# Kernel optimization log

Measured on AMD Instinct MI355X. Metric: run time of the kernel, lower is better.

The kernel has to match this reference:

```python
import jax, jax.numpy as jnp
import numpy as np

HID = 1024
HEADS = 16
HEAD_DIM = HID // HEADS
NEG = -10000000000.0


def setup_inputs() -> dict:
    key = jax.random.key(0)
    ks = jax.random.split(key, 12)
    B, S = 4, 2048
    scale = 1.0 / np.sqrt(HID)
    inp = {
        "query": jax.random.normal(ks[0], (B, S, HID), dtype=jnp.float32),
        "key": jax.random.normal(ks[1], (B, S, HID), dtype=jnp.float32),
        "value": jax.random.normal(ks[2], (B, S, HID), dtype=jnp.float32),
        "Wq": jax.random.normal(ks[3], (HID, HID), dtype=jnp.float32) * scale,
        "bq": jnp.zeros((HID,), dtype=jnp.float32),
        "Wk": jax.random.normal(ks[4], (HID, HID), dtype=jnp.float32) * scale,
        "bk": jnp.zeros((HID,), dtype=jnp.float32),
        "Wv": jax.random.normal(ks[5], (HID, HID), dtype=jnp.float32) * scale,
        "bv": jnp.zeros((HID,), dtype=jnp.float32),
        "Wo": jax.random.normal(ks[6], (HID, HID), dtype=jnp.float32) * scale,
        "bo": jnp.zeros((HID,), dtype=jnp.float32),
    }
    return inp


def reference(query, key, value, Wq, bq, Wk, bk, Wv, bv, Wo, bo):
    B, S, _ = query.shape
    # linear projections (nn.Linear: x @ W.T + b)
    q = query @ Wq.T + bq
    k = key @ Wk.T + bk
    v = value @ Wv.T + bv
    # split heads -> [B, H, S, D]
    q = q.reshape(B, S, HEADS, HEAD_DIM).transpose(0, 2, 1, 3)
    k = k.reshape(B, S, HEADS, HEAD_DIM).transpose(0, 2, 1, 3)
    v = v.reshape(B, S, HEADS, HEAD_DIM).transpose(0, 2, 1, 3)
    # NOTE: original module computes self.scale but never applies it -> unscaled logits
    attn = jnp.einsum("bhqd,bhkd->bhqk", q, k)
    causal = jnp.tril(jnp.ones((S, S), dtype=bool))
    attn = jnp.where(causal, attn, NEG)
    attn = jax.nn.softmax(attn, axis=-1)
    x = jnp.einsum("bhqk,bhkd->bhqd", attn, v)
    x = x.transpose(0, 2, 1, 3).reshape(B, S, HID)
    return x @ Wo.T + bo
```

## Files before the change

### kernel.cpp

```cpp
#include <hip/hip_runtime.h>
#include <hip/hip_fp16.h>

typedef _Float16 half_t;
typedef half_t halfx8 __attribute__((ext_vector_type(8)));
typedef half_t halfx4 __attribute__((ext_vector_type(4)));
typedef float floatx4 __attribute__((ext_vector_type(4)));

#define HID 1024
#define HEADS 16
#define HD 64
#define BATCH 4
#define SEQ 2048
#define MTOT (BATCH * SEQ)
#define NWELEM (HID * HID)

#define MFMA_F16 __builtin_amdgcn_mfma_f32_16x16x32_f16

__device__ inline halfx8 load8h(const half_t* p) { return *(const halfx8*)p; }
__device__ inline halfx8 load8h(const float* p) {
    floatx4 x = *(const floatx4*)p;
    floatx4 y = *(const floatx4*)(p + 4);
    halfx8 r;
    r[0] = (half_t)x[0]; r[1] = (half_t)x[1];
    r[2] = (half_t)x[2]; r[3] = (half_t)x[3];
    r[4] = (half_t)y[0]; r[5] = (half_t)y[1];
    r[6] = (half_t)y[2]; r[7] = (half_t)y[3];
    return r;
}

__device__ __forceinline__ void gl_lds16(const half_t* g, half_t* lds) {
    __builtin_amdgcn_global_load_lds(
        (const __attribute__((address_space(1))) void*)g,
        (__attribute__((address_space(3))) void*)lds, 16, 0, 0);
}

template <int MODE, typename TOut>
__device__ __forceinline__ void epilogue_store(
    const floatx4 (&acc)[4][4], const float* __restrict__ bias,
    TOut* __restrict__ Out, int m0, int n0, int wm, int wn, int quad, int l16)
{
    float bvals[4];
#pragma unroll
    for (int nt = 0; nt < 4; ++nt)
        bvals[nt] = bias[n0 + wn + nt * 16 + l16];

#pragma unroll
    for (int mt = 0; mt < 4; ++mt) {
        const int mbase = m0 + wm + mt * 16 + quad * 4;
#pragma unroll
        for (int nt = 0; nt < 4; ++nt) {
            const int n = n0 + wn + nt * 16 + l16;
            if (MODE == 2) {
                const int b = mbase >> 11, s = mbase & (SEQ - 1);
                const int h = n >> 6, d = n & (HD - 1);
                halfx4 st;
#pragma unroll
                for (int r = 0; r < 4; ++r)
                    st[r] = (half_t)(acc[mt][nt][r] + bvals[nt]);
                *(halfx4*)((half_t*)Out +
                    ((((size_t)b * HEADS + h) * HD + d) << 11) + s) = st;
            } else {
#pragma unroll
                for (int r = 0; r < 4; ++r) {
                    const float v = acc[mt][nt][r] + bvals[nt];
                    const int mm  = mbase + r;
                    if (MODE == 0) {
                        const int b = mm >> 11, s = mm & (SEQ - 1);
                        const int h = n >> 6, d = n & (HD - 1);
                        Out[((((size_t)b * HEADS + h) * SEQ + s) << 6) + d] = (TOut)v;
                    } else {
                        Out[(size_t)mm * HID + n] = (TOut)v;
                    }
                }
            }
        }
    }
}

template <int MODE, typename TOut>
__global__ __launch_bounds__(256) void gemm16(
    const half_t* __restrict__ A, const half_t* __restrict__ W,
    const float* __restrict__ bias, TOut* __restrict__ Out)
{
    __shared__ half_t As[128 * 32];
    __shared__ half_t Bs[128 * 32];

    const int tid  = threadIdx.x;
    const int m0   = blockIdx.y * 128;
    const int n0   = blockIdx.x * 128;
    const int wave = tid >> 6;
    const int lane = tid & 63;
    const int quad = lane >> 4;
    const int l16  = lane & 15;
    const int wm   = (wave >> 1) * 64;
    const int wn   = (wave & 1) * 64;

    const int c0   = wave * 2;
    const int srow = c0 * 16 + (lane >> 2);
    const int scol = (lane & 3) * 8;
    const half_t* aptr0 = A + (size_t)(m0 + srow) * HID + scol;
    const half_t* aptr1 = aptr0 + (size_t)16 * HID;
    const half_t* bptr0 = W + (size_t)(n0 + srow) * HID + scol;
    const half_t* bptr1 = bptr0 + (size_t)16 * HID;
    half_t* ldsA0 = &As[c0 * 512];
    half_t* ldsA1 = &As[c0 * 512 + 512];
    half_t* ldsB0 = &Bs[c0 * 512];
    half_t* ldsB1 = &Bs[c0 * 512 + 512];

    floatx4 acc[4][4];
    const floatx4 zero4 = {0.f, 0.f, 0.f, 0.f};
#pragma unroll
    for (int mt = 0; mt < 4; ++mt)
#pragma unroll
        for (int nt = 0; nt < 4; ++nt) acc[mt][nt] = zero4;

    for (int k0 = 0; k0 < HID; k0 += 32) {
        __syncthreads();
        gl_lds16(aptr0 + k0, ldsA0);
        gl_lds16(aptr1 + k0, ldsA1);
        gl_lds16(bptr0 + k0, ldsB0);
        gl_lds16(bptr1 + k0, ldsB1);
        __syncthreads();

        halfx8 af[4], bfr[4];
#pragma unroll
        for (int t = 0; t < 4; ++t) {
            af[t]  = *(const halfx8*)&As[(wm + t * 16 + l16) * 32 + quad * 8];
            bfr[t] = *(const halfx8*)&Bs[(wn + t * 16 + l16) * 32 + quad * 8];
        }
#pragma unroll
        for (int mt = 0; mt < 4; ++mt)
#pragma unroll
            for (int nt = 0; nt < 4; ++nt)
                acc[mt][nt] = MFMA_F16(af[mt], bfr[nt], acc[mt][nt], 0, 0, 0);
    }

    epilogue_store<MODE, TOut>(acc, bias, Out, m0, n0, wm, wn, quad, l16);
}

template <int MODE, typename TA, typename TOut>
__global__ __launch_bounds__(256) void gemm_bt(
    const TA* __restrict__ A, const float* __restrict__ W,
    const float* __restrict__ bias, TOut* __restrict__ Out)
{
    __shared__ half_t As[128][40];
    __shared__ half_t Bs[128][40];

    const int tid  = threadIdx.x;
    const int m0   = blockIdx.y * 128;
    const int n0   = blockIdx.x * 128;
    const int wave = tid >> 6;
    const int lane = tid & 63;
    const int quad = lane >> 4;
    const int l16  = lane & 15;
    const int wm   = (wave >> 1) * 64;
    const int wn   = (wave & 1) * 64;
    const int trow = tid >> 1;
    const int tcol = (tid & 1) * 16;

    const TA*    aptr = A + (size_t)(m0 + trow) * HID + tcol;
    const float* bptr = W + (size_t)(n0 + trow) * HID + tcol;

    floatx4 acc[4][4];
    const floatx4 zero4 = {0.f, 0.f, 0.f, 0.f};
#pragma unroll
    for (int mt = 0; mt < 4; ++mt)
#pragma unroll
        for (int nt = 0; nt < 4; ++nt) acc[mt][nt] = zero4;

    for (int k0 = 0; k0 < HID; k0 += 32) {
        halfx8 av0 = load8h(aptr);
        halfx8 av1 = load8h(aptr + 8);
        halfx8 bv0 = load8h(bptr);
        halfx8 bv1 = load8h(bptr + 8);
        aptr += 32;
        bptr += 32;

        __syncthreads();
        *(halfx8*)&As[trow][tcol]     = av0;
        *(halfx8*)&As[trow][tcol + 8] = av1;
        *(halfx8*)&Bs[trow][tcol]     = bv0;
        *(halfx8*)&Bs[trow][tcol + 8] = bv1;
        __syncthreads();

        halfx8 af[4], bfr[4];
#pragma unroll
        for (int t = 0; t < 4; ++t) {
            af[t]  = *(const halfx8*)&As[wm + t * 16 + l16][quad * 8];
            bfr[t] = *(const halfx8*)&Bs[wn + t * 16 + l16][quad * 8];
        }
#pragma unroll
        for (int mt = 0; mt < 4; ++mt)
#pragma unroll
            for (int nt = 0; nt < 4; ++nt)
                acc[mt][nt] = MFMA_F16(af[mt], bfr[nt], acc[mt][nt], 0, 0, 0);
    }

    epilogue_store<MODE, TOut>(acc, bias, Out, m0, n0, wm, wn, quad, l16);
}

__global__ __launch_bounds__(256) void cvt_act(
    const float* __restrict__ in, half_t* __restrict__ out)
{
    const size_t i = ((size_t)blockIdx.x * 256 + threadIdx.x) * 8;
    *(halfx8*)(out + i) = load8h(in + i);
}

__global__ __launch_bounds__(256) void cvt_w4(
    const float* __restrict__ w0, const float* __restrict__ w1,
    const float* __restrict__ w2, const float* __restrict__ w3,
    half_t* __restrict__ out)
{
    const int t = blockIdx.y;
    const float* src = (t == 0) ? w0 : (t == 1) ? w1 : (t == 2) ? w2 : w3;
    const size_t i = ((size_t)blockIdx.x * 256 + threadIdx.x) * 8;
    *(halfx8*)(out + (size_t)t * NWELEM + i) = load8h(src + i);
}

__global__ __launch_bounds__(256) void attn_kernel(
    const half_t* __restrict__ Q, const half_t* __restrict__ K,
    const half_t* __restrict__ VT, half_t* __restrict__ O)
{
    __shared__ half_t Ks[64][72];
    __shared__ half_t Vt[64][72];
    __shared__ half_t Pw[4][32][72];

    const int bh  = blockIdx.x;
    const int qt  = (gridDim.y - 1) - blockIdx.y;
    const int q0  = qt * 128;
    const int tid = threadIdx.x;
    const int wave = tid >> 6;
    const int lane = tid & 63;
    const int quad = lane >> 4;
    const int l16  = lane & 15;

    const half_t* Qb  = Q  + (size_t)bh * SEQ * HD;
    const half_t* Kb  = K  + (size_t)bh * SEQ * HD;
    const half_t* VTb = VT + (size_t)bh * HD * SEQ;

    halfx8 aq[2][2];
#pragma unroll
    for (int mt = 0; mt < 2; ++mt) {
        const half_t* p = Qb + (size_t)(q0 + wave * 32 + mt * 16 + l16) * HD + quad * 8;
        aq[mt][0] = *(const halfx8*)p;
        aq[mt][1] = *(const halfx8*)(p + 32);
    }

    const floatx4 zero4 = {0.f, 0.f, 0.f, 0.f};
    floatx4 oacc[2][4];
    float mrow[2][4], lrow[2][4];
#pragma unroll
    for (int mt = 0; mt < 2; ++mt)
#pragma unroll
        for (int i = 0; i < 4; ++i) {
            oacc[mt][i] = zero4;
            mrow[mt][i] = -3.0e38f;
            lrow[mt][i] = 0.f;
        }

    const int srow = tid >> 2;
    const int scol = (tid & 3) * 16;
    const int ktiles = 2 * qt + 2;

    for (int kt = 0; kt < ktiles; ++kt) {
        const int k0 = kt * 64;
        __syncthreads();
        {
            const half_t* ksrc = Kb + (size_t)(k0 + srow) * HD + scol;
            *(halfx8*)&Ks[srow][scol]     = *(const halfx8*)ksrc;
            *(halfx8*)&Ks[srow][scol + 8] = *(const halfx8*)(ksrc + 8);
            const half_t* vsrc = VTb + (size_t)srow * SEQ + k0 + scol;
            *(halfx8*)&Vt[srow][scol]     = *(const halfx8*)vsrc;
            *(halfx8*)&Vt[srow][scol + 8] = *(const halfx8*)(vsrc + 8);
        }
        __syncthreads();

        const bool active = (k0 <= q0 + wave * 32 + 31);

        if (active) {
            floatx4 sacc[2][4];
#pragma unroll
            for (int mt = 0; mt < 2; ++mt)
#pragma unroll
                for (int nt = 0; nt < 4; ++nt) sacc[mt][nt] = zero4;
#pragma unroll
            for (int nt = 0; nt < 4; ++nt) {
                halfx8 bk0 = *(const halfx8*)&Ks[nt * 16 + l16][quad * 8];
                halfx8 bk1 = *(const halfx8*)&Ks[nt * 16 + l16][quad * 8 + 32];
#pragma unroll
                for (int mt = 0; mt < 2; ++mt) {
                    sacc[mt][nt] = MFMA_F16(aq[mt][0], bk0, sacc[mt][nt], 0, 0, 0);
                    sacc[mt][nt] = MFMA_F16(aq[mt][1], bk1, sacc[mt][nt], 0, 0, 0);
                }
            }

            if (kt >= 2 * qt) {
#pragma unroll
                for (int mt = 0; mt < 2; ++mt)
#pragma unroll
                    for (int nt = 0; nt < 4; ++nt) {
                        const int kg = k0 + nt * 16 + l16;
#pragma unroll
                        for (int r = 0; r < 4; ++r) {
                            const int qg = q0 + wave * 32 + mt * 16 + quad * 4 + r;
                            if (kg > qg) sacc[mt][nt][r] = -1.0e30f;
                        }
                    }
            }

#pragma unroll
            for (int mt = 0; mt < 2; ++mt) {
                float alpha[4];
#pragma unroll
                for (int r = 0; r < 4; ++r) {
                    float mx = fmaxf(fmaxf(sacc[mt][0][r], sacc[mt][1][r]),
                                     fmaxf(sacc[mt][2][r], sacc[mt][3][r]));
                    mx = fmaxf(mx, __shfl_xor(mx, 1));
                    mx = fmaxf(mx, __shfl_xor(mx, 2));
                    mx = fmaxf(mx, __shfl_xor(mx, 4));
                    mx = fmaxf(mx, __shfl_xor(mx, 8));
                    const float mnew = fmaxf(mrow[mt][r], mx);
                    alpha[r]    = __expf(mrow[mt][r] - mnew);
                    mrow[mt][r] = mnew;
                }
                float rsum[4] = {0.f, 0.f, 0.f, 0.f};
#pragma unroll
                for (int nt = 0; nt < 4; ++nt)
#pragma unroll
                    for (int r = 0; r < 4; ++r) {
                        const float p = __expf(sacc[mt][nt][r] - mrow[mt][r]);
                        sacc[mt][nt][r] = p;
                        rsum[r] += p;
                    }
#pragma unroll
                for (int r = 0; r < 4; ++r) {
                    float s = rsum[r];
                    s += __shfl_xor(s, 1);
                    s += __shfl_xor(s, 2);
                    s += __shfl_xor(s, 4);
                    s += __shfl_xor(s, 8);
                    lrow[mt][r] = lrow[mt][r] * alpha[r] + s;
                }
#pragma unroll
                for (int dt = 0; dt < 4; ++dt)
#pragma unroll
                    for (int r = 0; r < 4; ++r) oacc[mt][dt][r] *= alpha[r];

#pragma unroll
                for (int nt = 0; nt < 4; ++nt)
#pragma unroll
                    for (int r = 0; r < 4; ++r)
                        Pw[wave][mt * 16 + quad * 4 + r][nt * 16 + l16] =
                            (half_t)sacc[mt][nt][r];
            }
        }

        __syncthreads();

        if (active) {
#pragma unroll
            for (int s2 = 0; s2 < 2; ++s2) {
                halfx8 ap0 = *(const halfx8*)&Pw[wave][l16][s2 * 32 + quad * 8];
                halfx8 ap1 = *(const halfx8*)&Pw[wave][16 + l16][s2 * 32 + quad * 8];
#pragma unroll
                for (int dt = 0; dt < 4; ++dt) {
                    halfx8 bv = *(const halfx8*)&Vt[dt * 16 + l16][s2 * 32 + quad * 8];
                    oacc[0][dt] = MFMA_F16(ap0, bv, oacc[0][dt], 0, 0, 0);
                    oacc[1][dt] = MFMA_F16(ap1, bv, oacc[1][dt], 0, 0, 0);
                }
            }
        }
    }

    const int b = bh >> 4, h = bh & (HEADS - 1);
#pragma unroll
    for (int mt = 0; mt < 2; ++mt)
#pragma unroll
        for (int dt = 0; dt < 4; ++dt)
#pragma unroll
            for (int r = 0; r < 4; ++r) {
                const int q = q0 + wave * 32 + mt * 16 + quad * 4 + r;
                const int d = h * HD + dt * 16 + l16;
                O[(size_t)(b * SEQ + q) * HID + d] =
                    (half_t)(oacc[mt][dt][r] / lrow[mt][r]);
            }
}

extern "C" void kernel_launch(void* const* d_in, const int* in_sizes, int n_in,
                              void* d_out, int out_size, void* d_ws, size_t ws_size,
                              hipStream_t stream)
{
    const float* query = (const float*)d_in[0];
    const float* key   = (const float*)d_in[1];
    const float* value = (const float*)d_in[2];
    const float* Wq    = (const float*)d_in[3];
    const float* bq    = (const float*)d_in[4];
    const float* Wk    = (const float*)d_in[5];
    const float* bk    = (const float*)d_in[6];
    const float* Wv    = (const float*)d_in[7];
    const float* bv    = (const float*)d_in[8];
    const float* Wo    = (const float*)d_in[9];
    const float* bo    = (const float*)d_in[10];
    float* out = (float*)d_out;

    const size_t NE = (size_t)MTOT * HID;
    half_t* Qp  = (half_t*)d_ws;
    half_t* Kp  = Qp  + NE;
    half_t* VpT = Kp  + NE;
    half_t* Ob  = VpT + NE;
    half_t* W16 = Ob  + NE;
    const size_t need = (4 * NE + 4 * (size_t)NWELEM) * sizeof(half_t);

    dim3 gg(HID / 128, MTOT / 128);
    dim3 ga(BATCH * HEADS, SEQ / 128);

    if (ws_size >= need) {
        half_t* act16 = Ob;
        const unsigned actBlocks = (unsigned)(NE / 2048);
        const unsigned wBlocks   = (unsigned)(NWELEM / 2048);

        cvt_w4<<<dim3(wBlocks, 4), 256, 0, stream>>>(Wq, Wk, Wv, Wo, W16);

        cvt_act<<<actBlocks, 256, 0, stream>>>(query, act16);
        gemm16<0, half_t><<<gg, 256, 0, stream>>>(act16, W16, bq, Qp);
        cvt_act<<<actBlocks, 256, 0, stream>>>(key, act16);
        gemm16<0, half_t><<<gg, 256, 0, stream>>>(act16, W16 + NWELEM, bk, Kp);
        cvt_act<<<actBlocks, 256, 0, stream>>>(value, act16);
        gemm16<2, half_t><<<gg, 256, 0, stream>>>(act16, W16 + 2 * (size_t)NWELEM, bv, VpT);

        attn_kernel<<<ga, 256, 0, stream>>>(Qp, Kp, VpT, Ob);

        gemm16<1, float><<<gg, 256, 0, stream>>>(Ob, W16 + 3 * (size_t)NWELEM, bo, out);
    } else {
        gemm_bt<0, float, half_t><<<gg, 256, 0, stream>>>(query, Wq, bq, Qp);
        gemm_bt<0, float, half_t><<<gg, 256, 0, stream>>>(key,   Wk, bk, Kp);
        gemm_bt<2, float, half_t><<<gg, 256, 0, stream>>>(value, Wv, bv, VpT);
        attn_kernel<<<ga, 256, 0, stream>>>(Qp, Kp, VpT, Ob);
        gemm_bt<1, half_t, float><<<gg, 256, 0, stream>>>(Ob, Wo, bo, out);
    }
}
```

Before: 408.5 us.

## Keep attention probabilities in registers via transposed MFMA and swizzle GEMM blocks

The attention kernel now computes S^T by swapping the MFMA operands, so each lane owns one query row. Row max and sum reductions then need only two cross-quad shuffles, and P is repacked into MFMA A-operand layout with register shuffles. This removes the per-tile LDS staging buffer and its extra __syncthreads, and the output is written with 4-wide vector stores. Separately, the GEMM remaps block IDs in groups of eight to improve L2 reuse; this mapping assumes 8 column tiles (gridDim.x == 8, i.e. N/128 = 8), which holds for 1024.

```diff
diff --git a/kernel.cpp b/kernel.cpp
--- a/kernel.cpp
+++ b/kernel.cpp
@@ -26,6 +26,12 @@
     r[4] = (half_t)y[0]; r[5] = (half_t)y[1];
     r[6] = (half_t)y[2]; r[7] = (half_t)y[3];
     return r;
+}
+
+__device__ __forceinline__ uint32_t pack2h(float a, float b) {
+    union { half_t h[2]; uint32_t u; } r;
+    r.h[0] = (half_t)a; r.h[1] = (half_t)b;
+    return r.u;
 }
 
 __device__ __forceinline__ void gl_lds16(const half_t* g, half_t* lds) {
@@ -86,8 +92,11 @@
     __shared__ half_t Bs[128 * 32];
 
     const int tid  = threadIdx.x;
-    const int m0   = blockIdx.y * 128;
-    const int n0   = blockIdx.x * 128;
+    const int id   = blockIdx.y * gridDim.x + blockIdx.x;
+    const int cpx  = (gridDim.x * gridDim.y) >> 3;
+    const int swz  = (id & 7) * cpx + (id >> 3);
+    const int m0   = (swz >> 3) * 128;
+    const int n0   = (swz & 7) * 128;
     const int wave = tid >> 6;
     const int lane = tid & 63;
     const int quad = lane >> 4;
@@ -223,7 +232,6 @@
 {
     __shared__ half_t Ks[64][72];
     __shared__ half_t Vt[64][72];
-    __shared__ half_t Pw[4][32][72];
 
     const int bh  = blockIdx.x;
     const int qt  = (gridDim.y - 1) - blockIdx.y;
@@ -247,20 +255,21 @@
     }
 
     const floatx4 zero4 = {0.f, 0.f, 0.f, 0.f};
-    floatx4 oacc[2][4];
-    float mrow[2][4], lrow[2][4];
-#pragma unroll
-    for (int mt = 0; mt < 2; ++mt)
-#pragma unroll
-        for (int i = 0; i < 4; ++i) {
-            oacc[mt][i] = zero4;
-            mrow[mt][i] = -3.0e38f;
-            lrow[mt][i] = 0.f;
-        }
+    floatx4 oaccT[2][4];
+    float mrow[2], lrow[2];
+#pragma unroll
+    for (int mt = 0; mt < 2; ++mt) {
+        mrow[mt] = -3.0e38f;
+        lrow[mt] = 0.f;
+#pragma unroll
+        for (int dt = 0; dt < 4; ++dt) oaccT[mt][dt] = zero4;
+    }
 
     const int srow = tid >> 2;
     const int scol = (tid & 3) * 16;
     const int ktiles = 2 * qt + 2;
+
+    union U8 { halfx8 h; uint32_t u[4]; };
 
     for (int kt = 0; kt < ktiles; ++kt) {
         const int k0 = kt * 64;
@@ -289,101 +298,101 @@
                 halfx8 bk1 = *(const halfx8*)&Ks[nt * 16 + l16][quad * 8 + 32];
 #pragma unroll
                 for (int mt = 0; mt < 2; ++mt) {
-                    sacc[mt][nt] = MFMA_F16(aq[mt][0], bk0, sacc[mt][nt], 0, 0, 0);
-                    sacc[mt][nt] = MFMA_F16(aq[mt][1], bk1, sacc[mt][nt], 0, 0, 0);
+                    sacc[mt][nt] = MFMA_F16(bk0, aq[mt][0], sacc[mt][nt], 0, 0, 0);
+                    sacc[mt][nt] = MFMA_F16(bk1, aq[mt][1], sacc[mt][nt], 0, 0, 0);
                 }
             }
 
             if (kt >= 2 * qt) {
 #pragma unroll
-                for (int mt = 0; mt < 2; ++mt)
+                for (int mt = 0; mt < 2; ++mt) {
+                    const int qg = q0 + wave * 32 + mt * 16 + l16;
 #pragma unroll
                     for (int nt = 0; nt < 4; ++nt) {
-                        const int kg = k0 + nt * 16 + l16;
-#pragma unroll
-                        for (int r = 0; r < 4; ++r) {
-                            const int qg = q0 + wave * 32 + mt * 16 + quad * 4 + r;
-                            if (kg > qg) sacc[mt][nt][r] = -1.0e30f;
-                        }
+                        const int kg = k0 + nt * 16 + quad * 4;
+#pragma unroll
+                        for (int r = 0; r < 4; ++r)
+                            if (kg + r > qg) sacc[mt][nt][r] = -1.0e30f;
                     }
+                }
             }
 
+            uint32_t pk[2][4][2];
 #pragma unroll
             for (int mt = 0; mt < 2; ++mt) {
-                float alpha[4];
-#pragma unroll
-                for (int r = 0; r < 4; ++r) {
-                    float mx = fmaxf(fmaxf(sacc[mt][0][r], sacc[mt][1][r]),
-                                     fmaxf(sacc[mt][2][r], sacc[mt][3][r]));
-                    mx = fmaxf(mx, __shfl_xor(mx, 1));
-                    mx = fmaxf(mx, __shfl_xor(mx, 2));
-                    mx = fmaxf(mx, __shfl_xor(mx, 4));
-                    mx = fmaxf(mx, __shfl_xor(mx, 8));
-                    const float mnew = fmaxf(mrow[mt][r], mx);
-                    alpha[r]    = __expf(mrow[mt][r] - mnew);
-                    mrow[mt][r] = mnew;
+                float mx = sacc[mt][0][0];
+#pragma unroll
+                for (int nt = 0; nt < 4; ++nt)
+#pragma unroll
+                    for (int r = 0; r < 4; ++r)
+                        if (nt | r) mx = fmaxf(mx, sacc[mt][nt][r]);
+                mx = fmaxf(mx, __shfl_xor(mx, 16));
+                mx = fmaxf(mx, __shfl_xor(mx, 32));
+                const float mnew  = fmaxf(mrow[mt], mx);
+                const float alpha = __expf(mrow[mt] - mnew);
+                mrow[mt] = mnew;
+
+                float rsum = 0.f;
+#pragma unroll
+                for (int nt = 0; nt < 4; ++nt)
+#pragma unroll
+                    for (int r = 0; r < 4; ++r) {
+                        const float p = __expf(sacc[mt][nt][r] - mnew);
+                        sacc[mt][nt][r] = p;
+                        rsum += p;
+                    }
+#pragma unroll
+                for (int nt = 0; nt < 4; ++nt) {
+                    pk[mt][nt][0] = pack2h(sacc[mt][nt][0], sacc[mt][nt][1]);
+                    pk[mt][nt][1] = pack2h(sacc[mt][nt][2], sacc[mt][nt][3]);
                 }
-                float rsum[4] = {0.f, 0.f, 0.f, 0.f};
-#pragma unroll
-                for (int nt = 0; nt < 4; ++nt)
-#pragma unroll
-                    for (int r = 0; r < 4; ++r) {
-                        const float p = __expf(sacc[mt][nt][r] - mrow[mt][r]);
-                        sacc[mt][nt][r] = p;
-                        rsum[r] += p;
+                rsum += __shfl_xor(rsum, 16);
+                rsum += __shfl_xor(rsum, 32);
+                lrow[mt] = lrow[mt] * alpha + rsum;
+#pragma unroll
+                for (int dt = 0; dt < 4; ++dt) oaccT[mt][dt] *= alpha;
+            }
+
+            U8 pb[2][2];
+#pragma unroll
+            for (int mt = 0; mt < 2; ++mt)
+#pragma unroll
+                for (int s2 = 0; s2 < 2; ++s2)
+#pragma unroll
+                    for (int w = 0; w < 4; ++w) {
+                        const int src = l16 + ((quad & 1) << 5) + ((w >> 1) << 4);
+                        const uint32_t lo =
+                            (uint32_t)__shfl((int)pk[mt][2 * s2][w & 1], src, 64);
+                        const uint32_t hi =
+                            (uint32_t)__shfl((int)pk[mt][2 * s2 + 1][w & 1], src, 64);
+                        pb[mt][s2].u[w] = (quad >> 1) ? hi : lo;
                     }
-#pragma unroll
-                for (int r = 0; r < 4; ++r) {
-                    float s = rsum[r];
-                    s += __shfl_xor(s, 1);
-                    s += __shfl_xor(s, 2);
-                    s += __shfl_xor(s, 4);
-                    s += __shfl_xor(s, 8);
-                    lrow[mt][r] = lrow[mt][r] * alpha[r] + s;
-                }
-#pragma unroll
-                for (int dt = 0; dt < 4; ++dt)
-#pragma unroll
-                    for (int r = 0; r < 4; ++r) oacc[mt][dt][r] *= alpha[r];
-
-#pragma unroll
-                for (int nt = 0; nt < 4; ++nt)
-#pragma unroll
-                    for (int r = 0; r < 4; ++r)
-                        Pw[wave][mt * 16 + quad * 4 + r][nt * 16 + l16] =
-                            (half_t)sacc[mt][nt][r];
-            }
-        }
-
-        __syncthreads();
-
-        if (active) {
-#pragma unroll
-            for (int s2 = 0; s2 < 2; ++s2) {
-                halfx8 ap0 = *(const halfx8*)&Pw[wave][l16][s2 * 32 + quad * 8];
-                halfx8 ap1 = *(const halfx8*)&Pw[wave][16 + l16][s2 * 32 + quad * 8];
+
+#pragma unroll
+            for (int s2 = 0; s2 < 2; ++s2)
 #pragma unroll
                 for (int dt = 0; dt < 4; ++dt) {
                     halfx8 bv = *(const halfx8*)&Vt[dt * 16 + l16][s2 * 32 + quad * 8];
-                    oacc[0][dt] = MFMA_F16(ap0, bv, oacc[0][dt], 0, 0, 0);
-                    oacc[1][dt] = MFMA_F16(ap1, bv, oacc[1][dt], 0, 0, 0);
+                    oaccT[0][dt] = MFMA_F16(bv, pb[0][s2].h, oaccT[0][dt], 0, 0, 0);
+                    oaccT[1][dt] = MFMA_F16(bv, pb[1][s2].h, oaccT[1][dt], 0, 0, 0);
                 }
-            }
         }
     }
 
     const int b = bh >> 4, h = bh & (HEADS - 1);
 #pragma unroll
-    for (int mt = 0; mt < 2; ++mt)
-#pragma unroll
-        for (int dt = 0; dt < 4; ++dt)
-#pragma unroll
-            for (int r = 0; r < 4; ++r) {
-                const int q = q0 + wave * 32 + mt * 16 + quad * 4 + r;
-                const int d = h * HD + dt * 16 + l16;
-                O[(size_t)(b * SEQ + q) * HID + d] =
-                    (half_t)(oacc[mt][dt][r] / lrow[mt][r]);
-            }
+    for (int mt = 0; mt < 2; ++mt) {
+        const int q = q0 + wave * 32 + mt * 16 + l16;
+#pragma unroll
+        for (int dt = 0; dt < 4; ++dt) {
+            halfx4 st;
+#pragma unroll
+            for (int r = 0; r < 4; ++r)
+                st[r] = (half_t)(oaccT[mt][dt][r] / lrow[mt]);
+            *(halfx4*)(O + (size_t)(b * SEQ + q) * HID +
+                       h * HD + dt * 16 + quad * 4) = st;
+        }
+    }
 }
 
 extern "C" void kernel_launch(void* const* d_in, const int* in_sizes, int n_in,
```

After: 362.1 us. -11.3%, faster.
